# Kernel tuning notes

Measured on AMD Instinct MI355X. Metric: run time of the kernel, lower is better.

Reference implementation:

```python
import jax, jax.numpy as jnp
import numpy as np

EPS = 1e-5  # torch LayerNorm default

def _layer_norm(x, g, b):
    m = jnp.mean(x, axis=-1, keepdims=True)
    v = jnp.mean((x - m) ** 2, axis=-1, keepdims=True)
    return (x - m) / jnp.sqrt(v + EPS) * g + b


def setup_inputs() -> dict:
    key = jax.random.key(0)
    ks = jax.random.split(key, 16)
    B, T, D, H = 2, 512, 256, 4
    dk = D // H
    s = 0.02
    p = lambda i, shape: jax.random.normal(ks[i], shape, jnp.float32) * s
    return {
        "x": jax.random.normal(ks[0], (B, T, D), jnp.float32),
        "r": jax.random.normal(ks[1], (B, T, T, D), jnp.float32),
        "mask": jnp.ones((B, 1, T, T), jnp.int32),
        "layer": 0,
        "info": 0,
        "Wq": p(2, (D, D)), "bq": jnp.zeros((D,), jnp.float32),
        "Wk": p(3, (D, D)), "bk": jnp.zeros((D,), jnp.float32),
        "Wv": p(4, (D, D)), "bv": jnp.zeros((D,), jnp.float32),
        "Wr": p(5, (D, D)), "br": jnp.zeros((D,), jnp.float32),
        "r_bias": p(6, (1, H, 1, dk)),
        "Wo": p(7, (D, D)), "bo": jnp.zeros((D,), jnp.float32),
        "g1": jnp.ones((D,), jnp.float32), "b1": jnp.zeros((D,), jnp.float32),
        "g2": jnp.ones((D,), jnp.float32), "b2": jnp.zeros((D,), jnp.float32),
        "W1": p(8, (D, 4 * D)), "fb1": jnp.zeros((4 * D,), jnp.float32),
        "W2": p(9, (4 * D, D)), "fb2": jnp.zeros((D,), jnp.float32),
    }


def reference(x, r, mask, layer, info,
              Wq, bq, Wk, bk, Wv, bv, Wr, br, r_bias, Wo, bo,
              g1, b1, g2, b2, W1, fb1, W2, fb2):
    B, T, D = x.shape
    H = r_bias.shape[1]
    dk = D // H
    scale = 1.0 / jnp.sqrt(jnp.float32(dk))

    # --- input sublayer: x + attention(LN(x)) (pre-norm residual) ---
    h = _layer_norm(x, g1, b1)
    q = (h @ Wq + bq).reshape(B, T, H, dk).transpose(0, 2, 1, 3)  # (B,H,T,dk)
    k = (h @ Wk + bk).reshape(B, T, H, dk).transpose(0, 2, 1, 3)
    v = (h @ Wv + bv).reshape(B, T, H, dk).transpose(0, 2, 1, 3)

    rr = (r @ Wr + br).reshape(B, T, T, H, dk).transpose(0, 3, 1, 2, 4)  # (B,H,T,T,dk)

    scores = jnp.einsum('bhid,bhjd->bhij', q, k)
    scores = scores + jnp.einsum('bhid,bhijd->bhij', q + r_bias, rr)
    scores = scores * scale
    scores = jnp.where(mask == 0, jnp.float32(-1e9), scores)
    p_attn = jax.nn.softmax(scores, axis=-1)
    attn = jnp.einsum('bhij,bhjd->bhid', p_attn, v)  # (B,H,T,dk)
    attn = attn.transpose(0, 2, 1, 3).reshape(B, T, D)
    attn = attn @ Wo + bo
    x = x + attn

    # --- output sublayer: x + FFN(LN(x)), gelu (exact), middle_drop=False ---
    h2 = _layer_norm(x, g2, b2)
    ffn = jax.nn.gelu(h2 @ W1 + fb1, approximate=False) @ W2 + fb2
    x = x + ffn
    return x
```

## Files before the change

### kernel.cpp

```cpp
#include <hip/hip_runtime.h>
#include <math.h>

constexpr int B_ = 2, T_ = 512, D_ = 256, H_ = 4, DK_ = 64;
constexpr int BT_ = B_ * T_;
constexpr int D4_ = 4 * D_;

#define F4E(v,i) ((i)==0?(v).x:((i)==1?(v).y:((i)==2?(v).z:(v).w)))

__global__ __launch_bounds__(256) void k_ln(const float* __restrict__ in,
                                            const float* __restrict__ g,
                                            const float* __restrict__ be,
                                            float* __restrict__ out) {
  int row = blockIdx.x, t = threadIdx.x, lane = t & 63, wid = t >> 6;
  __shared__ float red[4];
  float v = in[row * D_ + t];
  float s = v;
  #pragma unroll
  for (int o = 32; o > 0; o >>= 1) s += __shfl_xor(s, o, 64);
  if (lane == 0) red[wid] = s;
  __syncthreads();
  float mean = (red[0] + red[1] + red[2] + red[3]) * (1.0f / D_);
  float d = v - mean;
  float s2 = d * d;
  #pragma unroll
  for (int o = 32; o > 0; o >>= 1) s2 += __shfl_xor(s2, o, 64);
  __syncthreads();
  if (lane == 0) red[wid] = s2;
  __syncthreads();
  float var = (red[0] + red[1] + red[2] + red[3]) * (1.0f / D_);
  out[row * D_ + t] = d / sqrtf(var + 1e-5f) * g[t] + be[t];
}

__global__ __launch_bounds__(256) void k_qkv(const float* __restrict__ h,
    const float* __restrict__ Wq, const float* __restrict__ bq,
    const float* __restrict__ Wk, const float* __restrict__ bk,
    const float* __restrict__ Wv, const float* __restrict__ bv,
    float* __restrict__ q, float* __restrict__ k, float* __restrict__ v) {
  __shared__ float hs[8][D_];
  int t = threadIdx.x, row0 = blockIdx.x * 8;
  #pragma unroll
  for (int r = 0; r < 8; r++) hs[r][t] = h[(row0 + r) * D_ + t];
  __syncthreads();
  float qa[8], ka[8], va[8];
  float bqc = bq[t], bkc = bk[t], bvc = bv[t];
  #pragma unroll
  for (int r = 0; r < 8; r++) { qa[r] = bqc; ka[r] = bkc; va[r] = bvc; }
  for (int d = 0; d < D_; d += 4) {
    float4 hv[8];
    #pragma unroll
    for (int r = 0; r < 8; r++) hv[r] = *(const float4*)&hs[r][d];
    #pragma unroll
    for (int i = 0; i < 4; i++) {
      float wq = Wq[(d + i) * D_ + t], wk = Wk[(d + i) * D_ + t], wv = Wv[(d + i) * D_ + t];
      #pragma unroll
      for (int r = 0; r < 8; r++) {
        float hvv = F4E(hv[r], i);
        qa[r] = fmaf(hvv, wq, qa[r]);
        ka[r] = fmaf(hvv, wk, ka[r]);
        va[r] = fmaf(hvv, wv, va[r]);
      }
    }
  }
  int b = row0 / T_, hh = t >> 6, dd = t & 63;
  #pragma unroll
  for (int r = 0; r < 8; r++) {
    int tt = row0 + r - b * T_;
    size_t idx = ((size_t)(b * H_ + hh) * T_ + tt) * DK_ + dd;
    q[idx] = qa[r]; k[idx] = ka[r]; v[idx] = va[r];
  }
}

__global__ __launch_bounds__(256) void k_wbias(const float* __restrict__ q,
    const float* __restrict__ rbias, const float* __restrict__ Wr,
    const float* __restrict__ br, float* __restrict__ w, float* __restrict__ cq) {
  __shared__ float us[8][D_];
  int t = threadIdx.x, row0 = blockIdx.x * 8, b = row0 / T_;
  int hh = t >> 6, dd = t & 63;
  float rb = rbias[t];
  #pragma unroll
  for (int r = 0; r < 8; r++) {
    int tt = row0 + r - b * T_;
    us[r][t] = q[((size_t)(b * H_ + hh) * T_ + tt) * DK_ + dd] + rb;
  }
  __syncthreads();
  float acc[8][4];
  #pragma unroll
  for (int r = 0; r < 8; r++)
    #pragma unroll
    for (int h = 0; h < 4; h++) acc[r][h] = 0.0f;
  for (int h = 0; h < 4; h++) {
    for (int d4 = 0; d4 < 64; d4 += 4) {
      int cc = h * 64 + d4;
      float4 wr4 = *(const float4*)&Wr[(size_t)t * D_ + cc];
      #pragma unroll
      for (int r = 0; r < 8; r++) {
        float4 u4 = *(const float4*)&us[r][cc];
        acc[r][h] = fmaf(wr4.x, u4.x, fmaf(wr4.y, u4.y,
                    fmaf(wr4.z, u4.z, fmaf(wr4.w, u4.w, acc[r][h]))));
      }
    }
  }
  #pragma unroll
  for (int r = 0; r < 8; r++) {
    int bt = row0 + r;
    #pragma unroll
    for (int h = 0; h < 4; h++) w[(size_t)(bt * 4 + h) * D_ + t] = acc[r][h];
  }
  if (t < 32) {
    int r = t >> 2, h = t & 3;
    float s = 0;
    for (int d2 = 0; d2 < 64; d2++) s += us[r][h * 64 + d2] * br[h * 64 + d2];
    cq[(row0 + r) * 4 + h] = s;
  }
}

__global__ __launch_bounds__(256) void k_attn(const float* __restrict__ r,
    const int* __restrict__ mask, const float* __restrict__ q,
    const float* __restrict__ k, const float* __restrict__ v,
    const float* __restrict__ w, const float* __restrict__ cq,
    float* __restrict__ attn) {
  __shared__ float sw[H_ * D_];
  __shared__ float sq[D_];
  __shared__ float sc[H_][T_];
  __shared__ float scq[H_];
  __shared__ float sinv[H_];
  int t = threadIdx.x, bi = blockIdx.x;
  int b = bi >> 9, i = bi & (T_ - 1);
  #pragma unroll
  for (int u = 0; u < 4; u++) sw[u * 256 + t] = w[(size_t)bi * 1024 + u * 256 + t];
  sq[t] = q[((size_t)(b * H_ + (t >> 6)) * T_ + i) * DK_ + (t & 63)];
  if (t < 4) scq[t] = cq[bi * 4 + t];
  __syncthreads();

  float acc0[H_], acc1[H_];
  #pragma unroll
  for (int h = 0; h < H_; h++) { acc0[h] = 0; acc1[h] = 0; }

  #pragma unroll
  for (int jj = 0; jj < 2; jj++) {
    int j = t + jj * 256;
    #pragma unroll
    for (int h = 0; h < H_; h++) {
      const float4* kp = (const float4*)&k[((size_t)(b * H_ + h) * T_ + j) * DK_];
      const float4* qp = (const float4*)&sq[h * DK_];
      float s = 0;
      #pragma unroll
      for (int d4 = 0; d4 < 16; d4++) {
        float4 kv = kp[d4], qv = qp[d4];
        s = fmaf(kv.x, qv.x, s); s = fmaf(kv.y, qv.y, s);
        s = fmaf(kv.z, qv.z, s); s = fmaf(kv.w, qv.w, s);
      }
      if (jj == 0) acc0[h] = s; else acc1[h] = s;
    }
  }
  {
    const float4* rp0 = (const float4*)(r + ((size_t)(b * T_ + i) * T_ + t) * D_);
    const float4* rp1 = rp0 + (256 * D_) / 4;
    #pragma unroll 4
    for (int d4 = 0; d4 < 64; d4++) {
      float4 r0 = rp0[d4], r1 = rp1[d4];
      #pragma unroll
      for (int h = 0; h < H_; h++) {
        float4 wv = *(const float4*)&sw[h * D_ + 4 * d4];
        acc0[h] = fmaf(r0.x, wv.x, fmaf(r0.y, wv.y, fmaf(r0.z, wv.z, fmaf(r0.w, wv.w, acc0[h]))));
        acc1[h] = fmaf(r1.x, wv.x, fmaf(r1.y, wv.y, fmaf(r1.z, wv.z, fmaf(r1.w, wv.w, acc1[h]))));
      }
    }
  }
  const float scale = 0.125f;
  int mbase = (b * T_ + i) * T_;
  #pragma unroll
  for (int jj = 0; jj < 2; jj++) {
    int j = t + jj * 256;
    int mv = mask[mbase + j];
    #pragma unroll
    for (int h = 0; h < H_; h++) {
      float s = ((jj == 0 ? acc0[h] : acc1[h]) + scq[h]) * scale;
      if (mv == 0) s = -1e9f;
      sc[h][j] = s;
    }
  }
  __syncthreads();
  {
    int h = t >> 6, lane = t & 63;
    float vals[8];
    float m = -3.0e38f;
    #pragma unroll
    for (int kk = 0; kk < 8; kk++) { vals[kk] = sc[h][lane + 64 * kk]; m = fmaxf(m, vals[kk]); }
    #pragma unroll
    for (int o = 32; o > 0; o >>= 1) m = fmaxf(m, __shfl_xor(m, o, 64));
    float ss = 0;
    #pragma unroll
    for (int kk = 0; kk < 8; kk++) {
      float e = expf(vals[kk] - m);
      sc[h][lane + 64 * kk] = e;
      ss += e;
    }
    #pragma unroll
    for (int o = 32; o > 0; o >>= 1) ss += __shfl_xor(ss, o, 64);
    if (lane == 0) sinv[h] = 1.0f / ss;
  }
  __syncthreads();
  {
    int h = t >> 6, d = t & 63;
    const float* vp = &v[(size_t)(b * H_ + h) * T_ * DK_ + d];
    float a2 = 0;
    #pragma unroll 4
    for (int j = 0; j < T_; j += 4) {
      float4 p4 = *(const float4*)&sc[h][j];
      a2 = fmaf(p4.x, vp[(size_t)j * 64], a2);
      a2 = fmaf(p4.y, vp[(size_t)(j + 1) * 64], a2);
      a2 = fmaf(p4.z, vp[(size_t)(j + 2) * 64], a2);
      a2 = fmaf(p4.w, vp[(size_t)(j + 3) * 64], a2);
    }
    attn[(size_t)bi * D_ + t] = a2 * sinv[h];
  }
}

__global__ __launch_bounds__(256) void k_proj(const float* __restrict__ a,
    const float* __restrict__ Wo, const float* __restrict__ bo,
    const float* __restrict__ x, float* __restrict__ x1) {
  __shared__ float as[8][D_];
  int t = threadIdx.x, row0 = blockIdx.x * 8;
  #pragma unroll
  for (int r = 0; r < 8; r++) as[r][t] = a[(row0 + r) * D_ + t];
  __syncthreads();
  float acc[8];
  float bc = bo[t];
  #pragma unroll
  for (int r = 0; r < 8; r++) acc[r] = bc;
  for (int d = 0; d < D_; d += 4) {
    float4 av[8];
    #pragma unroll
    for (int r = 0; r < 8; r++) av[r] = *(const float4*)&as[r][d];
    #pragma unroll
    for (int i = 0; i < 4; i++) {
      float ww = Wo[(d + i) * D_ + t];
      #pragma unroll
      for (int r = 0; r < 8; r++) acc[r] = fmaf(F4E(av[r], i), ww, acc[r]);
    }
  }
  #pragma unroll
  for (int r = 0; r < 8; r++)
    x1[(row0 + r) * D_ + t] = x[(row0 + r) * D_ + t] + acc[r];
}

__global__ __launch_bounds__(256) void k_ffn1(const float* __restrict__ h2,
    const float* __restrict__ W1, const float* __restrict__ fb1,
    float* __restrict__ mid) {
  __shared__ float hs[8][D_];
  int t = threadIdx.x, row0 = blockIdx.x * 8;
  #pragma unroll
  for (int r = 0; r < 8; r++) hs[r][t] = h2[(row0 + r) * D_ + t];
  __syncthreads();
  float acc[8][4];
  #pragma unroll
  for (int c = 0; c < 4; c++) {
    float bb = fb1[t + c * 256];
    #pragma unroll
    for (int r = 0; r < 8; r++) acc[r][c] = bb;
  }
  for (int d = 0; d < D_; d += 4) {
    float4 hv[8];
    #pragma unroll
    for (int r = 0; r < 8; r++) hv[r] = *(const float4*)&hs[r][d];
    #pragma unroll
    for (int i = 0; i < 4; i++) {
      float wv[4];
      #pragma unroll
      for (int c = 0; c < 4; c++) wv[c] = W1[(size_t)(d + i) * D4_ + t + c * 256];
      #pragma unroll
      for (int r = 0; r < 8; r++) {
        float hvv = F4E(hv[r], i);
        #pragma unroll
        for (int c = 0; c < 4; c++) acc[r][c] = fmaf(hvv, wv[c], acc[r][c]);
      }
    }
  }
  #pragma unroll
  for (int r = 0; r < 8; r++)
    #pragma unroll
    for (int c = 0; c < 4; c++) {
      float val = acc[r][c];
      float ge = 0.5f * val * (1.0f + erff(val * 0.70710678118654752f));
      mid[(size_t)(row0 + r) * D4_ + t + c * 256] = ge;
    }
}

__global__ __launch_bounds__(256) void k_ffn2(const float* __restrict__ mid,
    const float* __restrict__ W2, const float* __restrict__ fb2,
    const float* __restrict__ x1, float* __restrict__ out) {
  __shared__ float ms[8][D4_];
  int t = threadIdx.x, row0 = blockIdx.x * 8;
  #pragma unroll
  for (int r = 0; r < 8; r++)
    #pragma unroll
    for (int c = 0; c < 4; c++)
      ms[r][t + c * 256] = mid[(size_t)(row0 + r) * D4_ + t + c * 256];
  __syncthreads();
  float acc[8];
  float bb = fb2[t];
  #pragma unroll
  for (int r = 0; r < 8; r++) acc[r] = bb;
  for (int d = 0; d < D4_; d += 4) {
    float4 mv[8];
    #pragma unroll
    for (int r = 0; r < 8; r++) mv[r] = *(const float4*)&ms[r][d];
    #pragma unroll
    for (int i = 0; i < 4; i++) {
      float ww = W2[(size_t)(d + i) * D_ + t];
      #pragma unroll
      for (int r = 0; r < 8; r++) acc[r] = fmaf(F4E(mv[r], i), ww, acc[r]);
    }
  }
  #pragma unroll
  for (int r = 0; r < 8; r++)
    out[(row0 + r) * D_ + t] = x1[(row0 + r) * D_ + t] + acc[r];
}

extern "C" void kernel_launch(void* const* d_in, const int* in_sizes, int n_in,
                              void* d_out, int out_size, void* d_ws, size_t ws_size,
                              hipStream_t stream) {
  const float* x     = (const float*)d_in[0];
  const float* r     = (const float*)d_in[1];
  const int*   mask  = (const int*)d_in[2];
  const float* Wq = (const float*)d_in[5];  const float* bq = (const float*)d_in[6];
  const float* Wk = (const float*)d_in[7];  const float* bk = (const float*)d_in[8];
  const float* Wv = (const float*)d_in[9];  const float* bv = (const float*)d_in[10];
  const float* Wr = (const float*)d_in[11]; const float* br = (const float*)d_in[12];
  const float* rbias = (const float*)d_in[13];
  const float* Wo = (const float*)d_in[14]; const float* bo = (const float*)d_in[15];
  const float* g1 = (const float*)d_in[16]; const float* b1 = (const float*)d_in[17];
  const float* g2 = (const float*)d_in[18]; const float* b2 = (const float*)d_in[19];
  const float* W1 = (const float*)d_in[20]; const float* fb1 = (const float*)d_in[21];
  const float* W2 = (const float*)d_in[22]; const float* fb2 = (const float*)d_in[23];
  float* out = (float*)d_out;

  float* ws = (float*)d_ws;
  float* h1b   = ws;
  float* qb    = ws + 262144;
  float* kb    = ws + 524288;
  float* vb    = ws + 786432;
  float* wb    = ws + 1048576;
  float* cqb   = ws + 2097152;
  float* attnb = ws + 2101248;
  float* x1b   = ws + 2363392;
  float* h2b   = ws + 2625536;
  float* midb  = ws + 2887680;

  k_ln  <<<BT_,     256, 0, stream>>>(x, g1, b1, h1b);
  k_qkv <<<BT_ / 8, 256, 0, stream>>>(h1b, Wq, bq, Wk, bk, Wv, bv, qb, kb, vb);
  k_wbias<<<BT_ / 8,256, 0, stream>>>(qb, rbias, Wr, br, wb, cqb);
  k_attn<<<BT_,     256, 0, stream>>>(r, mask, qb, kb, vb, wb, cqb, attnb);
  k_proj<<<BT_ / 8, 256, 0, stream>>>(attnb, Wo, bo, x, x1b);
  k_ln  <<<BT_,     256, 0, stream>>>(x1b, g2, b2, h2b);
  k_ffn1<<<BT_ / 8, 256, 0, stream>>>(h2b, W1, fb1, midb);
  k_ffn2<<<BT_ / 8, 256, 0, stream>>>(midb, W2, fb2, x1b, out);
}
```

Before: 1.054 ms.

## Fuse pipeline into three kernels and restructure attention r-stream loads

Replaces the eight-kernel pipeline with three. The first fuses LayerNorm, the QKV projection and the relative-position weight precompute. The second fuses the attention scores, softmax, AV product, output projection, residual and second LayerNorm. The third fuses both FFN matmuls with GELU and keeps the intermediate in shared memory. The attention kernel now reads r rows cooperatively: 16 lanes per row with float4 loads, double-buffered register prefetch and shuffle reductions, replacing the old per-thread strided row reads. This removes launches and intermediate HBM round trips, but halves the rows per block in the GEMM kernels, which lowers weight reuse, and switches LayerNorm to a one-pass variance.

```diff
diff --git a/kernel.cpp b/kernel.cpp
--- a/kernel.cpp
+++ b/kernel.cpp
@@ -7,315 +7,311 @@
 
 #define F4E(v,i) ((i)==0?(v).x:((i)==1?(v).y:((i)==2?(v).z:(v).w)))
 
-__global__ __launch_bounds__(256) void k_ln(const float* __restrict__ in,
-                                            const float* __restrict__ g,
-                                            const float* __restrict__ be,
-                                            float* __restrict__ out) {
-  int row = blockIdx.x, t = threadIdx.x, lane = t & 63, wid = t >> 6;
-  __shared__ float red[4];
-  float v = in[row * D_ + t];
-  float s = v;
-  #pragma unroll
-  for (int o = 32; o > 0; o >>= 1) s += __shfl_xor(s, o, 64);
-  if (lane == 0) red[wid] = s;
-  __syncthreads();
-  float mean = (red[0] + red[1] + red[2] + red[3]) * (1.0f / D_);
-  float d = v - mean;
-  float s2 = d * d;
-  #pragma unroll
-  for (int o = 32; o > 0; o >>= 1) s2 += __shfl_xor(s2, o, 64);
-  __syncthreads();
-  if (lane == 0) red[wid] = s2;
-  __syncthreads();
-  float var = (red[0] + red[1] + red[2] + red[3]) * (1.0f / D_);
-  out[row * D_ + t] = d / sqrtf(var + 1e-5f) * g[t] + be[t];
-}
-
-__global__ __launch_bounds__(256) void k_qkv(const float* __restrict__ h,
+__device__ __forceinline__ float dot4(float4 a, float4 b) {
+  return fmaf(a.x, b.x, fmaf(a.y, b.y, fmaf(a.z, b.z, a.w * b.w)));
+}
+
+__global__ __launch_bounds__(256) void k1_ln_qkv_w(
+    const float* __restrict__ x,
+    const float* __restrict__ g1, const float* __restrict__ b1,
     const float* __restrict__ Wq, const float* __restrict__ bq,
     const float* __restrict__ Wk, const float* __restrict__ bk,
     const float* __restrict__ Wv, const float* __restrict__ bv,
-    float* __restrict__ q, float* __restrict__ k, float* __restrict__ v) {
-  __shared__ float hs[8][D_];
-  int t = threadIdx.x, row0 = blockIdx.x * 8;
-  #pragma unroll
-  for (int r = 0; r < 8; r++) hs[r][t] = h[(row0 + r) * D_ + t];
-  __syncthreads();
-  float qa[8], ka[8], va[8];
-  float bqc = bq[t], bkc = bk[t], bvc = bv[t];
-  #pragma unroll
-  for (int r = 0; r < 8; r++) { qa[r] = bqc; ka[r] = bkc; va[r] = bvc; }
+    const float* __restrict__ rbias, const float* __restrict__ Wr,
+    const float* __restrict__ br,
+    float* __restrict__ q, float* __restrict__ k, float* __restrict__ v,
+    float* __restrict__ w, float* __restrict__ cq) {
+  __shared__ float hs[4][D_];
+  __shared__ float us[4][D_];
+  int t = threadIdx.x, lane = t & 63, wid = t >> 6;
+  int row0 = blockIdx.x * 4, b = row0 >> 9;
+
+  {
+    const float* xr = x + (size_t)(row0 + wid) * D_;
+    float v0 = xr[lane], v1 = xr[lane + 64], v2 = xr[lane + 128], v3 = xr[lane + 192];
+    float s = v0 + v1 + v2 + v3;
+    float s2 = fmaf(v0, v0, fmaf(v1, v1, fmaf(v2, v2, v3 * v3)));
+    #pragma unroll
+    for (int o = 32; o > 0; o >>= 1) { s += __shfl_xor(s, o, 64); s2 += __shfl_xor(s2, o, 64); }
+    float m = s * (1.0f / D_);
+    float var = s2 * (1.0f / D_) - m * m;
+    float rinv = rsqrtf(var + 1e-5f);
+    hs[wid][lane]       = (v0 - m) * rinv * g1[lane]       + b1[lane];
+    hs[wid][lane + 64]  = (v1 - m) * rinv * g1[lane + 64]  + b1[lane + 64];
+    hs[wid][lane + 128] = (v2 - m) * rinv * g1[lane + 128] + b1[lane + 128];
+    hs[wid][lane + 192] = (v3 - m) * rinv * g1[lane + 192] + b1[lane + 192];
+  }
+  __syncthreads();
+
+  float qa[4], ka[4], va[4];
+  {
+    float bqc = bq[t], bkc = bk[t], bvc = bv[t];
+    #pragma unroll
+    for (int r2 = 0; r2 < 4; r2++) { qa[r2] = bqc; ka[r2] = bkc; va[r2] = bvc; }
+  }
   for (int d = 0; d < D_; d += 4) {
-    float4 hv[8];
-    #pragma unroll
-    for (int r = 0; r < 8; r++) hv[r] = *(const float4*)&hs[r][d];
+    float4 h4[4];
+    #pragma unroll
+    for (int r2 = 0; r2 < 4; r2++) h4[r2] = *(const float4*)&hs[r2][d];
     #pragma unroll
     for (int i = 0; i < 4; i++) {
-      float wq = Wq[(d + i) * D_ + t], wk = Wk[(d + i) * D_ + t], wv = Wv[(d + i) * D_ + t];
+      float wqv = Wq[(d + i) * D_ + t], wkv = Wk[(d + i) * D_ + t], wvv = Wv[(d + i) * D_ + t];
       #pragma unroll
-      for (int r = 0; r < 8; r++) {
-        float hvv = F4E(hv[r], i);
-        qa[r] = fmaf(hvv, wq, qa[r]);
-        ka[r] = fmaf(hvv, wk, ka[r]);
-        va[r] = fmaf(hvv, wv, va[r]);
+      for (int r2 = 0; r2 < 4; r2++) {
+        float hv = F4E(h4[r2], i);
+        qa[r2] = fmaf(hv, wqv, qa[r2]);
+        ka[r2] = fmaf(hv, wkv, ka[r2]);
+        va[r2] = fmaf(hv, wvv, va[r2]);
       }
     }
   }
-  int b = row0 / T_, hh = t >> 6, dd = t & 63;
-  #pragma unroll
-  for (int r = 0; r < 8; r++) {
-    int tt = row0 + r - b * T_;
-    size_t idx = ((size_t)(b * H_ + hh) * T_ + tt) * DK_ + dd;
-    q[idx] = qa[r]; k[idx] = ka[r]; v[idx] = va[r];
-  }
-}
-
-__global__ __launch_bounds__(256) void k_wbias(const float* __restrict__ q,
-    const float* __restrict__ rbias, const float* __restrict__ Wr,
-    const float* __restrict__ br, float* __restrict__ w, float* __restrict__ cq) {
-  __shared__ float us[8][D_];
-  int t = threadIdx.x, row0 = blockIdx.x * 8, b = row0 / T_;
   int hh = t >> 6, dd = t & 63;
   float rb = rbias[t];
   #pragma unroll
-  for (int r = 0; r < 8; r++) {
-    int tt = row0 + r - b * T_;
-    us[r][t] = q[((size_t)(b * H_ + hh) * T_ + tt) * DK_ + dd] + rb;
-  }
-  __syncthreads();
-  float acc[8][4];
-  #pragma unroll
-  for (int r = 0; r < 8; r++)
-    #pragma unroll
-    for (int h = 0; h < 4; h++) acc[r][h] = 0.0f;
-  for (int h = 0; h < 4; h++) {
-    for (int d4 = 0; d4 < 64; d4 += 4) {
-      int cc = h * 64 + d4;
-      float4 wr4 = *(const float4*)&Wr[(size_t)t * D_ + cc];
+  for (int r2 = 0; r2 < 4; r2++) {
+    int tt = (row0 & 511) + r2;
+    size_t idx = ((size_t)(b * H_ + hh) * T_ + tt) * DK_ + dd;
+    q[idx] = qa[r2]; k[idx] = ka[r2]; v[idx] = va[r2];
+    us[r2][t] = qa[r2] + rb;
+  }
+  __syncthreads();
+
+  float acc[4][4];
+  #pragma unroll
+  for (int r2 = 0; r2 < 4; r2++) {
+    #pragma unroll
+    for (int h2 = 0; h2 < 4; h2++) acc[r2][h2] = 0.0f;
+  }
+  const float4* wr4 = (const float4*)&Wr[(size_t)t * D_];
+  #pragma unroll
+  for (int h2 = 0; h2 < 4; h2++) {
+    #pragma unroll 4
+    for (int d4 = 0; d4 < 16; d4++) {
+      float4 wv4 = wr4[h2 * 16 + d4];
       #pragma unroll
-      for (int r = 0; r < 8; r++) {
-        float4 u4 = *(const float4*)&us[r][cc];
-        acc[r][h] = fmaf(wr4.x, u4.x, fmaf(wr4.y, u4.y,
-                    fmaf(wr4.z, u4.z, fmaf(wr4.w, u4.w, acc[r][h]))));
+      for (int r2 = 0; r2 < 4; r2++) {
+        float4 u4 = *(const float4*)&us[r2][h2 * 64 + d4 * 4];
+        acc[r2][h2] = fmaf(wv4.x, u4.x, fmaf(wv4.y, u4.y,
+                       fmaf(wv4.z, u4.z, fmaf(wv4.w, u4.w, acc[r2][h2]))));
       }
     }
   }
   #pragma unroll
-  for (int r = 0; r < 8; r++) {
-    int bt = row0 + r;
-    #pragma unroll
-    for (int h = 0; h < 4; h++) w[(size_t)(bt * 4 + h) * D_ + t] = acc[r][h];
-  }
-  if (t < 32) {
-    int r = t >> 2, h = t & 3;
+  for (int r2 = 0; r2 < 4; r2++) {
+    #pragma unroll
+    for (int h2 = 0; h2 < 4; h2++)
+      w[(size_t)((row0 + r2) * 4 + h2) * D_ + t] = acc[r2][h2];
+  }
+  if (t < 16) {
+    int r2 = t >> 2, h2 = t & 3;
     float s = 0;
-    for (int d2 = 0; d2 < 64; d2++) s += us[r][h * 64 + d2] * br[h * 64 + d2];
-    cq[(row0 + r) * 4 + h] = s;
-  }
-}
-
-__global__ __launch_bounds__(256) void k_attn(const float* __restrict__ r,
-    const int* __restrict__ mask, const float* __restrict__ q,
-    const float* __restrict__ k, const float* __restrict__ v,
-    const float* __restrict__ w, const float* __restrict__ cq,
-    float* __restrict__ attn) {
+    for (int d2 = 0; d2 < 64; d2++) s = fmaf(us[r2][h2 * 64 + d2], br[h2 * 64 + d2], s);
+    cq[(row0 + r2) * 4 + h2] = s;
+  }
+}
+
+__global__ __launch_bounds__(256) void k2_attn(
+    const float* __restrict__ r, const int* __restrict__ mask,
+    const float* __restrict__ q, const float* __restrict__ k,
+    const float* __restrict__ v, const float* __restrict__ w,
+    const float* __restrict__ cq, const float* __restrict__ x,
+    const float* __restrict__ Wo, const float* __restrict__ bo,
+    const float* __restrict__ g2, const float* __restrict__ b2,
+    float* __restrict__ x1, float* __restrict__ h2o) {
   __shared__ float sw[H_ * D_];
   __shared__ float sq[D_];
   __shared__ float sc[H_][T_];
+  __shared__ float ar[D_];
   __shared__ float scq[H_];
-  __shared__ float sinv[H_];
-  int t = threadIdx.x, bi = blockIdx.x;
-  int b = bi >> 9, i = bi & (T_ - 1);
+  __shared__ float redA[4], redB[4];
+  int t = threadIdx.x, lane = t & 63, wid = t >> 6, qt = lane & 15;
+  int bi = blockIdx.x, b = bi >> 9, i = bi & (T_ - 1);
+
   #pragma unroll
   for (int u = 0; u < 4; u++) sw[u * 256 + t] = w[(size_t)bi * 1024 + u * 256 + t];
-  sq[t] = q[((size_t)(b * H_ + (t >> 6)) * T_ + i) * DK_ + (t & 63)];
+  sq[t] = q[((size_t)(b * H_ + wid) * T_ + i) * DK_ + lane];
   if (t < 4) scq[t] = cq[bi * 4 + t];
   __syncthreads();
 
-  float acc0[H_], acc1[H_];
-  #pragma unroll
-  for (int h = 0; h < H_; h++) { acc0[h] = 0; acc1[h] = 0; }
-
-  #pragma unroll
-  for (int jj = 0; jj < 2; jj++) {
-    int j = t + jj * 256;
-    #pragma unroll
-    for (int h = 0; h < H_; h++) {
-      const float4* kp = (const float4*)&k[((size_t)(b * H_ + h) * T_ + j) * DK_];
-      const float4* qp = (const float4*)&sq[h * DK_];
-      float s = 0;
-      #pragma unroll
-      for (int d4 = 0; d4 < 16; d4++) {
-        float4 kv = kp[d4], qv = qp[d4];
-        s = fmaf(kv.x, qv.x, s); s = fmaf(kv.y, qv.y, s);
-        s = fmaf(kv.z, qv.z, s); s = fmaf(kv.w, qv.w, s);
-      }
-      if (jj == 0) acc0[h] = s; else acc1[h] = s;
-    }
-  }
+  float4 wreg[4][4];
+  float4 qreg[4];
+  #pragma unroll
+  for (int h = 0; h < 4; h++) {
+    qreg[h] = *(const float4*)&sq[h * 64 + 4 * qt];
+    #pragma unroll
+    for (int u = 0; u < 4; u++)
+      wreg[h][u] = *(const float4*)&sw[h * 256 + 64 * u + 4 * qt];
+  }
+
+  const float* rbase = r + (size_t)bi * (T_ * D_);
+  const float* kbase = k + (size_t)b * (H_ * T_ * DK_);
+  int rowoff = lane >> 4;
+  float4 rA[4], kA[4];
+  float4 rB[4] = {}, kB[4] = {};
+
+  auto loadR = [&](int it, float4* rr) {
+    int jr = wid * 128 + it * 4 + rowoff;
+    const float4* rp = (const float4*)(rbase + (size_t)jr * D_);
+    rr[0] = rp[qt]; rr[1] = rp[16 + qt]; rr[2] = rp[32 + qt]; rr[3] = rp[48 + qt];
+  };
+  auto loadK = [&](int it, float4* kk2) {
+    int jr = wid * 128 + it * 4 + rowoff;
+    #pragma unroll
+    for (int h = 0; h < 4; h++)
+      kk2[h] = *(const float4*)(kbase + ((size_t)h * T_ + jr) * DK_ + 4 * qt);
+  };
+
+  loadR(0, rA); loadK(0, kA);
+  for (int it = 0; it < 32; ++it) {
+    if (it < 31) { loadR(it + 1, rB); loadK(it + 1, kB); }
+    float p0 = dot4(kA[0], qreg[0]) + dot4(rA[0], wreg[0][0]) + dot4(rA[1], wreg[0][1])
+             + dot4(rA[2], wreg[0][2]) + dot4(rA[3], wreg[0][3]);
+    float p1 = dot4(kA[1], qreg[1]) + dot4(rA[0], wreg[1][0]) + dot4(rA[1], wreg[1][1])
+             + dot4(rA[2], wreg[1][2]) + dot4(rA[3], wreg[1][3]);
+    float p2 = dot4(kA[2], qreg[2]) + dot4(rA[0], wreg[2][0]) + dot4(rA[1], wreg[2][1])
+             + dot4(rA[2], wreg[2][2]) + dot4(rA[3], wreg[2][3]);
+    float p3 = dot4(kA[3], qreg[3]) + dot4(rA[0], wreg[3][0]) + dot4(rA[1], wreg[3][1])
+             + dot4(rA[2], wreg[3][2]) + dot4(rA[3], wreg[3][3]);
+    #pragma unroll
+    for (int off = 1; off <= 8; off <<= 1) {
+      p0 += __shfl_xor(p0, off, 64);
+      p1 += __shfl_xor(p1, off, 64);
+      p2 += __shfl_xor(p2, off, 64);
+      p3 += __shfl_xor(p3, off, 64);
+    }
+    if (qt < 4) {
+      int jr = wid * 128 + it * 4 + rowoff;
+      float val = (qt == 0) ? p0 : (qt == 1) ? p1 : (qt == 2) ? p2 : p3;
+      float s = (val + scq[qt]) * 0.125f;
+      if (mask[(size_t)bi * T_ + jr] == 0) s = -1e9f;
+      sc[qt][jr] = s;
+    }
+    #pragma unroll
+    for (int u = 0; u < 4; u++) { rA[u] = rB[u]; kA[u] = kB[u]; }
+  }
+  __syncthreads();
+
   {
-    const float4* rp0 = (const float4*)(r + ((size_t)(b * T_ + i) * T_ + t) * D_);
-    const float4* rp1 = rp0 + (256 * D_) / 4;
-    #pragma unroll 4
-    for (int d4 = 0; d4 < 64; d4++) {
-      float4 r0 = rp0[d4], r1 = rp1[d4];
-      #pragma unroll
-      for (int h = 0; h < H_; h++) {
-        float4 wv = *(const float4*)&sw[h * D_ + 4 * d4];
-        acc0[h] = fmaf(r0.x, wv.x, fmaf(r0.y, wv.y, fmaf(r0.z, wv.z, fmaf(r0.w, wv.w, acc0[h]))));
-        acc1[h] = fmaf(r1.x, wv.x, fmaf(r1.y, wv.y, fmaf(r1.z, wv.z, fmaf(r1.w, wv.w, acc1[h]))));
-      }
-    }
-  }
-  const float scale = 0.125f;
-  int mbase = (b * T_ + i) * T_;
-  #pragma unroll
-  for (int jj = 0; jj < 2; jj++) {
-    int j = t + jj * 256;
-    int mv = mask[mbase + j];
-    #pragma unroll
-    for (int h = 0; h < H_; h++) {
-      float s = ((jj == 0 ? acc0[h] : acc1[h]) + scq[h]) * scale;
-      if (mv == 0) s = -1e9f;
-      sc[h][j] = s;
-    }
-  }
-  __syncthreads();
-  {
-    int h = t >> 6, lane = t & 63;
     float vals[8];
     float m = -3.0e38f;
     #pragma unroll
-    for (int kk = 0; kk < 8; kk++) { vals[kk] = sc[h][lane + 64 * kk]; m = fmaxf(m, vals[kk]); }
+    for (int kk2 = 0; kk2 < 8; kk2++) { vals[kk2] = sc[wid][lane + 64 * kk2]; m = fmaxf(m, vals[kk2]); }
     #pragma unroll
     for (int o = 32; o > 0; o >>= 1) m = fmaxf(m, __shfl_xor(m, o, 64));
     float ss = 0;
     #pragma unroll
-    for (int kk = 0; kk < 8; kk++) {
-      float e = expf(vals[kk] - m);
-      sc[h][lane + 64 * kk] = e;
+    for (int kk2 = 0; kk2 < 8; kk2++) {
+      float e = expf(vals[kk2] - m);
+      sc[wid][lane + 64 * kk2] = e;
       ss += e;
     }
     #pragma unroll
     for (int o = 32; o > 0; o >>= 1) ss += __shfl_xor(ss, o, 64);
-    if (lane == 0) sinv[h] = 1.0f / ss;
-  }
-  __syncthreads();
-  {
-    int h = t >> 6, d = t & 63;
-    const float* vp = &v[(size_t)(b * H_ + h) * T_ * DK_ + d];
+    float inv = 1.0f / ss;
+
+    const float* vp = v + (size_t)(b * H_ + wid) * T_ * DK_ + lane;
     float a2 = 0;
     #pragma unroll 4
     for (int j = 0; j < T_; j += 4) {
-      float4 p4 = *(const float4*)&sc[h][j];
+      float4 p4 = *(const float4*)&sc[wid][j];
       a2 = fmaf(p4.x, vp[(size_t)j * 64], a2);
       a2 = fmaf(p4.y, vp[(size_t)(j + 1) * 64], a2);
       a2 = fmaf(p4.z, vp[(size_t)(j + 2) * 64], a2);
       a2 = fmaf(p4.w, vp[(size_t)(j + 3) * 64], a2);
     }
-    attn[(size_t)bi * D_ + t] = a2 * sinv[h];
-  }
-}
-
-__global__ __launch_bounds__(256) void k_proj(const float* __restrict__ a,
-    const float* __restrict__ Wo, const float* __restrict__ bo,
-    const float* __restrict__ x, float* __restrict__ x1) {
-  __shared__ float as[8][D_];
-  int t = threadIdx.x, row0 = blockIdx.x * 8;
-  #pragma unroll
-  for (int r = 0; r < 8; r++) as[r][t] = a[(row0 + r) * D_ + t];
-  __syncthreads();
-  float acc[8];
-  float bc = bo[t];
-  #pragma unroll
-  for (int r = 0; r < 8; r++) acc[r] = bc;
-  for (int d = 0; d < D_; d += 4) {
-    float4 av[8];
-    #pragma unroll
-    for (int r = 0; r < 8; r++) av[r] = *(const float4*)&as[r][d];
-    #pragma unroll
-    for (int i = 0; i < 4; i++) {
-      float ww = Wo[(d + i) * D_ + t];
+    ar[t] = a2 * inv;
+  }
+  __syncthreads();
+
+  float acc = bo[t];
+  #pragma unroll 4
+  for (int d4 = 0; d4 < 64; d4++) {
+    float4 a4 = *(const float4*)&ar[4 * d4];
+    acc = fmaf(a4.x, Wo[(4 * d4 + 0) * D_ + t], acc);
+    acc = fmaf(a4.y, Wo[(4 * d4 + 1) * D_ + t], acc);
+    acc = fmaf(a4.z, Wo[(4 * d4 + 2) * D_ + t], acc);
+    acc = fmaf(a4.w, Wo[(4 * d4 + 3) * D_ + t], acc);
+  }
+  float x1v = x[(size_t)bi * D_ + t] + acc;
+  float s1 = x1v, s2v = x1v * x1v;
+  #pragma unroll
+  for (int o = 32; o > 0; o >>= 1) { s1 += __shfl_xor(s1, o, 64); s2v += __shfl_xor(s2v, o, 64); }
+  if (lane == 0) { redA[wid] = s1; redB[wid] = s2v; }
+  __syncthreads();
+  float mm = (redA[0] + redA[1] + redA[2] + redA[3]) * (1.0f / D_);
+  float var = (redB[0] + redB[1] + redB[2] + redB[3]) * (1.0f / D_) - mm * mm;
+  float rinv = rsqrtf(var + 1e-5f);
+  x1[(size_t)bi * D_ + t] = x1v;
+  h2o[(size_t)bi * D_ + t] = (x1v - mm) * rinv * g2[t] + b2[t];
+}
+
+__global__ __launch_bounds__(256) void k3_ffn(
+    const float* __restrict__ h2, const float* __restrict__ W1,
+    const float* __restrict__ fb1, const float* __restrict__ W2,
+    const float* __restrict__ fb2, const float* __restrict__ x1,
+    float* __restrict__ out) {
+  __shared__ float hs[4][D_];
+  __shared__ float ms[4][D4_];
+  int t = threadIdx.x, row0 = blockIdx.x * 4;
+  #pragma unroll
+  for (int r2 = 0; r2 < 4; r2++) hs[r2][t] = h2[(size_t)(row0 + r2) * D_ + t];
+  __syncthreads();
+
+  float acc[4][4];
+  #pragma unroll
+  for (int c = 0; c < 4; c++) {
+    float bb = fb1[t + 256 * c];
+    #pragma unroll
+    for (int r2 = 0; r2 < 4; r2++) acc[r2][c] = bb;
+  }
+  for (int d4 = 0; d4 < 64; d4++) {
+    float4 h4[4];
+    #pragma unroll
+    for (int r2 = 0; r2 < 4; r2++) h4[r2] = *(const float4*)&hs[r2][4 * d4];
+    #pragma unroll
+    for (int i2 = 0; i2 < 4; i2++) {
+      float wv0 = W1[(size_t)(4 * d4 + i2) * D4_ + t];
+      float wv1 = W1[(size_t)(4 * d4 + i2) * D4_ + t + 256];
+      float wv2 = W1[(size_t)(4 * d4 + i2) * D4_ + t + 512];
+      float wv3 = W1[(size_t)(4 * d4 + i2) * D4_ + t + 768];
       #pragma unroll
-      for (int r = 0; r < 8; r++) acc[r] = fmaf(F4E(av[r], i), ww, acc[r]);
-    }
-  }
-  #pragma unroll
-  for (int r = 0; r < 8; r++)
-    x1[(row0 + r) * D_ + t] = x[(row0 + r) * D_ + t] + acc[r];
-}
-
-__global__ __launch_bounds__(256) void k_ffn1(const float* __restrict__ h2,
-    const float* __restrict__ W1, const float* __restrict__ fb1,
-    float* __restrict__ mid) {
-  __shared__ float hs[8][D_];
-  int t = threadIdx.x, row0 = blockIdx.x * 8;
-  #pragma unroll
-  for (int r = 0; r < 8; r++) hs[r][t] = h2[(row0 + r) * D_ + t];
-  __syncthreads();
-  float acc[8][4];
-  #pragma unroll
-  for (int c = 0; c < 4; c++) {
-    float bb = fb1[t + c * 256];
-    #pragma unroll
-    for (int r = 0; r < 8; r++) acc[r][c] = bb;
-  }
-  for (int d = 0; d < D_; d += 4) {
-    float4 hv[8];
-    #pragma unroll
-    for (int r = 0; r < 8; r++) hv[r] = *(const float4*)&hs[r][d];
-    #pragma unroll
-    for (int i = 0; i < 4; i++) {
-      float wv[4];
+      for (int r2 = 0; r2 < 4; r2++) {
+        float hv = F4E(h4[r2], i2);
+        acc[r2][0] = fmaf(hv, wv0, acc[r2][0]);
+        acc[r2][1] = fmaf(hv, wv1, acc[r2][1]);
+        acc[r2][2] = fmaf(hv, wv2, acc[r2][2]);
+        acc[r2][3] = fmaf(hv, wv3, acc[r2][3]);
+      }
+    }
+  }
+  #pragma unroll
+  for (int r2 = 0; r2 < 4; r2++) {
+    #pragma unroll
+    for (int c = 0; c < 4; c++) {
+      float val = acc[r2][c];
+      ms[r2][t + 256 * c] = 0.5f * val * (1.0f + erff(val * 0.70710678118654752f));
+    }
+  }
+  __syncthreads();
+
+  float a2[4];
+  float bb2 = fb2[t];
+  #pragma unroll
+  for (int r2 = 0; r2 < 4; r2++) a2[r2] = bb2;
+  for (int d4 = 0; d4 < 256; d4++) {
+    float4 m4[4];
+    #pragma unroll
+    for (int r2 = 0; r2 < 4; r2++) m4[r2] = *(const float4*)&ms[r2][4 * d4];
+    #pragma unroll
+    for (int i2 = 0; i2 < 4; i2++) {
+      float wv = W2[(size_t)(4 * d4 + i2) * D_ + t];
       #pragma unroll
-      for (int c = 0; c < 4; c++) wv[c] = W1[(size_t)(d + i) * D4_ + t + c * 256];
-      #pragma unroll
-      for (int r = 0; r < 8; r++) {
-        float hvv = F4E(hv[r], i);
-        #pragma unroll
-        for (int c = 0; c < 4; c++) acc[r][c] = fmaf(hvv, wv[c], acc[r][c]);
-      }
-    }
-  }
-  #pragma unroll
-  for (int r = 0; r < 8; r++)
-    #pragma unroll
-    for (int c = 0; c < 4; c++) {
-      float val = acc[r][c];
-      float ge = 0.5f * val * (1.0f + erff(val * 0.70710678118654752f));
-      mid[(size_t)(row0 + r) * D4_ + t + c * 256] = ge;
-    }
-}
-
-__global__ __launch_bounds__(256) void k_ffn2(const float* __restrict__ mid,
-    const float* __restrict__ W2, const float* __restrict__ fb2,
-    const float* __restrict__ x1, float* __restrict__ out) {
-  __shared__ float ms[8][D4_];
-  int t = threadIdx.x, row0 = blockIdx.x * 8;
-  #pragma unroll
-  for (int r = 0; r < 8; r++)
-    #pragma unroll
-    for (int c = 0; c < 4; c++)
-      ms[r][t + c * 256] = mid[(size_t)(row0 + r) * D4_ + t + c * 256];
-  __syncthreads();
-  float acc[8];
-  float bb = fb2[t];
-  #pragma unroll
-  for (int r = 0; r < 8; r++) acc[r] = bb;
-  for (int d = 0; d < D4_; d += 4) {
-    float4 mv[8];
-    #pragma unroll
-    for (int r = 0; r < 8; r++) mv[r] = *(const float4*)&ms[r][d];
-    #pragma unroll
-    for (int i = 0; i < 4; i++) {
-      float ww = W2[(size_t)(d + i) * D_ + t];
-      #pragma unroll
-      for (int r = 0; r < 8; r++) acc[r] = fmaf(F4E(mv[r], i), ww, acc[r]);
-    }
-  }
-  #pragma unroll
-  for (int r = 0; r < 8; r++)
-    out[(row0 + r) * D_ + t] = x1[(row0 + r) * D_ + t] + acc[r];
+      for (int r2 = 0; r2 < 4; r2++) a2[r2] = fmaf(F4E(m4[r2], i2), wv, a2[r2]);
+    }
+  }
+  #pragma unroll
+  for (int r2 = 0; r2 < 4; r2++)
+    out[(size_t)(row0 + r2) * D_ + t] = x1[(size_t)(row0 + r2) * D_ + t] + a2[r2];
 }
 
 extern "C" void kernel_launch(void* const* d_in, const int* in_sizes, int n_in,
@@ -337,23 +333,17 @@
   float* out = (float*)d_out;
 
   float* ws = (float*)d_ws;
-  float* h1b   = ws;
-  float* qb    = ws + 262144;
-  float* kb    = ws + 524288;
-  float* vb    = ws + 786432;
-  float* wb    = ws + 1048576;
-  float* cqb   = ws + 2097152;
-  float* attnb = ws + 2101248;
-  float* x1b   = ws + 2363392;
-  float* h2b   = ws + 2625536;
-  float* midb  = ws + 2887680;
-
-  k_ln  <<<BT_,     256, 0, stream>>>(x, g1, b1, h1b);
-  k_qkv <<<BT_ / 8, 256, 0, stream>>>(h1b, Wq, bq, Wk, bk, Wv, bv, qb, kb, vb);
-  k_wbias<<<BT_ / 8,256, 0, stream>>>(qb, rbias, Wr, br, wb, cqb);
-  k_attn<<<BT_,     256, 0, stream>>>(r, mask, qb, kb, vb, wb, cqb, attnb);
-  k_proj<<<BT_ / 8, 256, 0, stream>>>(attnb, Wo, bo, x, x1b);
-  k_ln  <<<BT_,     256, 0, stream>>>(x1b, g2, b2, h2b);
-  k_ffn1<<<BT_ / 8, 256, 0, stream>>>(h2b, W1, fb1, midb);
-  k_ffn2<<<BT_ / 8, 256, 0, stream>>>(midb, W2, fb2, x1b, out);
-}
+  float* qb  = ws;
+  float* kb  = ws + 262144;
+  float* vb  = ws + 524288;
+  float* wb  = ws + 786432;
+  float* cqb = ws + 1835008;
+  float* x1b = ws + 1839104;
+  float* h2b = ws + 2101248;
+
+  k1_ln_qkv_w<<<BT_ / 4, 256, 0, stream>>>(x, g1, b1, Wq, bq, Wk, bk, Wv, bv,
+                                           rbias, Wr, br, qb, kb, vb, wb, cqb);
+  k2_attn<<<BT_, 256, 0, stream>>>(r, mask, qb, kb, vb, wb, cqb, x,
+                                   Wo, bo, g2, b2, x1b, h2b);
+  k3_ffn<<<BT_ / 4, 256, 0, stream>>>(h2b, W1, fb1, W2, fb2, x1b, out);
+}
```

After: 880.5 us. -16.5%, faster.
